# Kernel optimization log

Hardware: AMD Instinct MI355X
Metric: run time of the kernel (lower is better)

## Reference

```python
import jax, jax.numpy as jnp
import numpy as np

BATCH, CHANNELS, SIZE = 32, 2048, 4096


def setup_inputs() -> dict:
    key = jax.random.key(0)
    kx, kw = jax.random.split(key)
    x = jax.random.normal(kx, (BATCH, CHANNELS, SIZE), dtype=jnp.float32)
    # xavier_uniform for weights [channels, size]
    limit = float(np.sqrt(6.0 / (CHANNELS + SIZE)))
    weights = jax.random.uniform(kw, (CHANNELS, SIZE), dtype=jnp.float32,
                                 minval=-limit, maxval=limit)
    bias = jnp.zeros((SIZE,), dtype=jnp.float32)
    return {"x": x, "weights": weights, "bias": bias}


def reference(x, weights, bias):
    # diagonal(sample.T @ W)[j] = sum_c sample[c, j] * W[c, j]
    # -> channelwise dot-product, vectorized over batch; avoids the
    #    wasteful full [size, size] matmul of the original.
    diag = jnp.einsum('bcs,cs->bs', x, weights)  # [batch, size]
    return jax.nn.relu(diag + bias)
```

## Files before the change

kernel.cpp:

```cpp
#include <hip/hip_runtime.h>

#define BATCH    32
#define CHANNELS 2048
#define SIZE     4096

constexpr int BX  = 64;
constexpr int BY  = 8;
constexpr int VEC = 4;
constexpr int S_PER_BLOCK = BX * VEC;
constexpr int C_PER_Y     = CHANNELS / BY;

__global__ __launch_bounds__(BX * BY)
void CWG_82214263980322_kernel(const float* __restrict__ x,
                               const float* __restrict__ w,
                               const float* __restrict__ bias,
                               float* __restrict__ out)
{
    __shared__ float4 smem[BY][BX];

    const int tx = threadIdx.x;
    const int ty = threadIdx.y;
    const int s_tile = blockIdx.x;
    const int b = blockIdx.y;

    const int s = s_tile * S_PER_BLOCK + tx * VEC;

    const float4* xp = reinterpret_cast<const float4*>(
        x + (size_t)b * CHANNELS * SIZE + (size_t)ty * C_PER_Y * SIZE + s);
    const float4* wp = reinterpret_cast<const float4*>(
        w + (size_t)ty * C_PER_Y * SIZE + s);

    float4 acc = make_float4(0.f, 0.f, 0.f, 0.f);

    #pragma unroll 8
    for (int c = 0; c < C_PER_Y; ++c) {
        const float4 xv = xp[(size_t)c * (SIZE / VEC)];
        const float4 wv = wp[(size_t)c * (SIZE / VEC)];
        acc.x = fmaf(xv.x, wv.x, acc.x);
        acc.y = fmaf(xv.y, wv.y, acc.y);
        acc.z = fmaf(xv.z, wv.z, acc.z);
        acc.w = fmaf(xv.w, wv.w, acc.w);
    }

    smem[ty][tx] = acc;
    __syncthreads();

    if (ty == 0) {
        float4 t = smem[0][tx];
        #pragma unroll
        for (int j = 1; j < BY; ++j) {
            const float4 u = smem[j][tx];
            t.x += u.x; t.y += u.y; t.z += u.z; t.w += u.w;
        }
        const float4 bv = *reinterpret_cast<const float4*>(bias + s);
        t.x = fmaxf(t.x + bv.x, 0.f);
        t.y = fmaxf(t.y + bv.y, 0.f);
        t.z = fmaxf(t.z + bv.z, 0.f);
        t.w = fmaxf(t.w + bv.w, 0.f);
        *reinterpret_cast<float4*>(out + (size_t)b * SIZE + s) = t;
    }
}

extern "C" void kernel_launch(void* const* d_in, const int* in_sizes, int n_in,
                              void* d_out, int out_size, void* d_ws, size_t ws_size,
                              hipStream_t stream) {
    const float* x    = (const float*)d_in[0];
    const float* w    = (const float*)d_in[1];
    const float* bias = (const float*)d_in[2];
    float* out        = (float*)d_out;

    dim3 grid(SIZE / S_PER_BLOCK, BATCH);
    dim3 block(BX, BY);
    CWG_82214263980322_kernel<<<grid, block, 0, stream>>>(x, w, bias, out);
}
```

Baseline: 1.332 ms.

## Split channel reduction across blocks, reuse weights over four batches

Each thread now loads one weight vector and applies it to four batch rows, which cuts weight traffic. The channel dimension is split into 8 chunks across blocks, and the partial sums are written to workspace. A second kernel adds the partials, then applies bias and ReLU. x is read with nontemporal loads to avoid polluting the cache. The costs are an extra launch and extra partial-sum traffic, both small next to the 1 GB x stream.

```diff
diff --git a/kernel.cpp b/kernel.cpp
--- a/kernel.cpp
+++ b/kernel.cpp
@@ -4,61 +4,86 @@
 #define CHANNELS 2048
 #define SIZE     4096
 
-constexpr int BX  = 64;
-constexpr int BY  = 8;
-constexpr int VEC = 4;
-constexpr int S_PER_BLOCK = BX * VEC;
-constexpr int C_PER_Y     = CHANNELS / BY;
+typedef float v4f __attribute__((ext_vector_type(4)));
+
+constexpr int BX    = 64;
+constexpr int BY    = 4;
+constexpr int NB    = 4;
+constexpr int CCH   = 8;
+constexpr int CBLK  = CHANNELS / CCH;
+constexpr int CW    = CBLK / BY;
+constexpr int SPB   = BX * 4;
+constexpr int STILES = SIZE / SPB;
+constexpr int BG    = BATCH / NB;
+constexpr int TILES = STILES * CCH;
 
 __global__ __launch_bounds__(BX * BY)
-void CWG_82214263980322_kernel(const float* __restrict__ x,
-                               const float* __restrict__ w,
-                               const float* __restrict__ bias,
-                               float* __restrict__ out)
+void CWG_k1(const float* __restrict__ x,
+            const float* __restrict__ w,
+            float* __restrict__ partial)
 {
-    __shared__ float4 smem[BY][BX];
+    __shared__ v4f smem[NB][BY][BX];
 
     const int tx = threadIdx.x;
     const int ty = threadIdx.y;
-    const int s_tile = blockIdx.x;
-    const int b = blockIdx.y;
+    const int id = blockIdx.x;
+    const int bg   = id / TILES;
+    const int tile = id % TILES;
+    const int cc   = tile / STILES;
+    const int st   = tile % STILES;
 
-    const int s = s_tile * S_PER_BLOCK + tx * VEC;
+    const int s  = st * SPB + tx * 4;
+    const int c0 = cc * CBLK + ty * CW;
+    const int b0 = bg * NB;
 
-    const float4* xp = reinterpret_cast<const float4*>(
-        x + (size_t)b * CHANNELS * SIZE + (size_t)ty * C_PER_Y * SIZE + s);
-    const float4* wp = reinterpret_cast<const float4*>(
-        w + (size_t)ty * C_PER_Y * SIZE + s);
+    const float* wp = w + (size_t)c0 * SIZE + s;
+    const float* xp = x + ((size_t)b0 * CHANNELS + (size_t)c0) * SIZE + s;
 
-    float4 acc = make_float4(0.f, 0.f, 0.f, 0.f);
+    v4f acc[NB];
+    #pragma unroll
+    for (int nb = 0; nb < NB; ++nb) acc[nb] = (v4f)(0.f);
 
-    #pragma unroll 8
-    for (int c = 0; c < C_PER_Y; ++c) {
-        const float4 xv = xp[(size_t)c * (SIZE / VEC)];
-        const float4 wv = wp[(size_t)c * (SIZE / VEC)];
-        acc.x = fmaf(xv.x, wv.x, acc.x);
-        acc.y = fmaf(xv.y, wv.y, acc.y);
-        acc.z = fmaf(xv.z, wv.z, acc.z);
-        acc.w = fmaf(xv.w, wv.w, acc.w);
+    #pragma unroll 4
+    for (int c = 0; c < CW; ++c) {
+        const v4f wv = *reinterpret_cast<const v4f*>(wp + (size_t)c * SIZE);
+        #pragma unroll
+        for (int nb = 0; nb < NB; ++nb) {
+            const v4f xv = __builtin_nontemporal_load(
+                reinterpret_cast<const v4f*>(
+                    xp + ((size_t)nb * CHANNELS + (size_t)c) * SIZE));
+            acc[nb] = xv * wv + acc[nb];
+        }
     }
 
-    smem[ty][tx] = acc;
+    #pragma unroll
+    for (int nb = 0; nb < NB; ++nb) smem[nb][ty][tx] = acc[nb];
     __syncthreads();
 
-    if (ty == 0) {
-        float4 t = smem[0][tx];
-        #pragma unroll
-        for (int j = 1; j < BY; ++j) {
-            const float4 u = smem[j][tx];
-            t.x += u.x; t.y += u.y; t.z += u.z; t.w += u.w;
-        }
-        const float4 bv = *reinterpret_cast<const float4*>(bias + s);
-        t.x = fmaxf(t.x + bv.x, 0.f);
-        t.y = fmaxf(t.y + bv.y, 0.f);
-        t.z = fmaxf(t.z + bv.z, 0.f);
-        t.w = fmaxf(t.w + bv.w, 0.f);
-        *reinterpret_cast<float4*>(out + (size_t)b * SIZE + s) = t;
-    }
+    v4f t = smem[ty][0][tx] + smem[ty][1][tx] + smem[ty][2][tx] + smem[ty][3][tx];
+    const int b = b0 + ty;
+    *reinterpret_cast<v4f*>(partial + ((size_t)cc * BATCH + b) * SIZE + s) = t;
+}
+
+__global__ __launch_bounds__(256)
+void CWG_k2(const float* __restrict__ partial,
+            const float* __restrict__ bias,
+            float* __restrict__ out)
+{
+    const int t  = blockIdx.x * blockDim.x + threadIdx.x;
+    const int b  = t >> 10;
+    const int s  = (t & 1023) * 4;
+
+    v4f sum = *reinterpret_cast<const v4f*>(bias + s);
+    #pragma unroll
+    for (int cc = 0; cc < CCH; ++cc)
+        sum += *reinterpret_cast<const v4f*>(partial + ((size_t)cc * BATCH + b) * SIZE + s);
+
+    v4f r;
+    r.x = fmaxf(sum.x, 0.f);
+    r.y = fmaxf(sum.y, 0.f);
+    r.z = fmaxf(sum.z, 0.f);
+    r.w = fmaxf(sum.w, 0.f);
+    *reinterpret_cast<v4f*>(out + (size_t)b * SIZE + s) = r;
 }
 
 extern "C" void kernel_launch(void* const* d_in, const int* in_sizes, int n_in,
@@ -68,8 +93,10 @@
     const float* w    = (const float*)d_in[1];
     const float* bias = (const float*)d_in[2];
     float* out        = (float*)d_out;
+    float* partial    = (float*)d_ws;
 
-    dim3 grid(SIZE / S_PER_BLOCK, BATCH);
-    dim3 block(BX, BY);
-    CWG_82214263980322_kernel<<<grid, block, 0, stream>>>(x, w, bias, out);
+    CWG_k1<<<dim3(BG * TILES), dim3(BX, BY), 0, stream>>>(x, w, partial);
+
+    const int n2 = BATCH * SIZE / 4;
+    CWG_k2<<<dim3(n2 / 256), dim3(256), 0, stream>>>(partial, bias, out);
 }
```

Measured after the change: 1.331 ms. Within noise of the previous version (-0.1%).
